# Performance work log

Hardware: AMD Instinct MI355X
Metric: run time of the kernel (lower is better)

The kernel has to match this reference:

```python
import jax, jax.numpy as jnp
import numpy as np

B, S, D, H = 2, 2048, 1024, 16
HD = D // H

def setup_inputs() -> dict:
    key = jax.random.key(0)
    ks = jax.random.split(key, 12)
    std = 1.0 / np.sqrt(D)
    query = jax.random.normal(ks[0], (B, S, D), jnp.float32)
    kk = jax.random.normal(ks[1], (B, S, D), jnp.float32)
    vv = jax.random.normal(ks[2], (B, S, D), jnp.float32)
    # per-batch valid lengths; True = padded position
    lengths = jax.random.randint(ks[3], (B,), S // 2, S + 1)
    key_padding_mask = jnp.arange(S)[None, :] >= lengths[:, None]
    Wq = jax.random.uniform(ks[4], (D, D), jnp.float32, -std, std)
    bq = jnp.zeros((D,), jnp.float32)
    Wk = jax.random.uniform(ks[5], (D, D), jnp.float32, -std, std)
    bk = jnp.zeros((D,), jnp.float32)
    Wv = jax.random.uniform(ks[6], (D, D), jnp.float32, -std, std)
    bv = jnp.zeros((D,), jnp.float32)
    Wo = jax.random.uniform(ks[7], (D, D), jnp.float32, -std, std)
    bo = jnp.zeros((D,), jnp.float32)
    return {"query": query, "key": kk, "value": vv,
            "key_padding_mask": key_padding_mask,
            "Wq": Wq, "bq": bq, "Wk": Wk, "bk": bk,
            "Wv": Wv, "bv": bv, "Wo": Wo, "bo": bo}

def reference(query, key, value, key_padding_mask, Wq, bq, Wk, bk, Wv, bv, Wo, bo):
    scale = HD ** -0.5
    # projections -> [B, H, S, HD]
    def proj(x, W, b):
        return (x @ W.T + b).reshape(B, S, H, HD).transpose(0, 2, 1, 3)
    q = proj(query, Wq, bq)
    k = proj(key, Wk, bk)
    v = proj(value, Wv, bv)
    scores = jnp.einsum('bhqd,bhkd->bhqk', q, k) * scale  # [B,H,S,S]
    pos = jnp.arange(S)
    rel_bias = -0.1 * jnp.abs(pos[:, None] - pos[None, :]).astype(scores.dtype)
    scores = scores + rel_bias[None, None]
    scores = jnp.where(key_padding_mask[:, None, None, :], -jnp.inf, scores)
    attn = jax.nn.softmax(scores, axis=-1)  # dropout is identity in eval
    out = jnp.einsum('bhqk,bhkd->bhqd', attn, v)
    out = out.transpose(0, 2, 1, 3).reshape(B, S, D)
    return out @ Wo.T + bo
```

## Files before the change

kernel.cpp:

```cpp
#include <hip/hip_runtime.h>

typedef __attribute__((ext_vector_type(8))) short bf16x8;
typedef __attribute__((ext_vector_type(4))) short s16x4;
typedef __attribute__((ext_vector_type(8))) short s16x8;
typedef __attribute__((ext_vector_type(4))) float fx4;
typedef __attribute__((ext_vector_type(2))) unsigned int u32x2;

static __device__ __forceinline__ short f2bf(float f) {
  unsigned u = __builtin_bit_cast(unsigned, f);
  u += 0x7fffu + ((u >> 16) & 1u);
  return (short)(u >> 16);
}

static __device__ __forceinline__ void gload_lds16(const void* g, void* l) {
  __builtin_amdgcn_global_load_lds(
      (const __attribute__((address_space(1))) unsigned int*)g,
      (__attribute__((address_space(3))) unsigned int*)l, 16, 0, 0);
}

#define BB_ 2
#define SS_ 2048
#define DD_ 1024
#define HH_ 16
#define HD_ 64

__global__ __launch_bounds__(256) void cvt_kernel(
    const float* __restrict__ q, const float* __restrict__ k, const float* __restrict__ v,
    const float* __restrict__ Wq, const float* __restrict__ Wk, const float* __restrict__ Wv,
    const float* __restrict__ Wo,
    short* __restrict__ xq, short* __restrict__ xk, short* __restrict__ xv,
    short* __restrict__ wq, short* __restrict__ wk, short* __restrict__ wv,
    short* __restrict__ wo) {
  size_t e = ((size_t)blockIdx.x * 256 + threadIdx.x) * 8;
  const float* src; short* dst; size_t off;
  if (e < 4194304u)        { src = q;  dst = xq; off = e; }
  else if (e < 8388608u)   { src = k;  dst = xk; off = e - 4194304u; }
  else if (e < 12582912u)  { src = v;  dst = xv; off = e - 8388608u; }
  else if (e < 13631488u)  { src = Wq; dst = wq; off = e - 12582912u; }
  else if (e < 14680064u)  { src = Wk; dst = wk; off = e - 13631488u; }
  else if (e < 15728640u)  { src = Wv; dst = wv; off = e - 14680064u; }
  else                     { src = Wo; dst = wo; off = e - 15728640u; }
  fx4 a = *(const fx4*)(src + off);
  fx4 b = *(const fx4*)(src + off + 4);
  s16x8 o;
  o[0] = f2bf(a[0]); o[1] = f2bf(a[1]); o[2] = f2bf(a[2]); o[3] = f2bf(a[3]);
  o[4] = f2bf(b[0]); o[5] = f2bf(b[1]); o[6] = f2bf(b[2]); o[7] = f2bf(b[3]);
  *(s16x8*)(dst + off) = o;
}

__global__ __launch_bounds__(256) void proj_gemm(
    const short* __restrict__ xq, const short* __restrict__ xk, const short* __restrict__ xv,
    const short* __restrict__ wq, const short* __restrict__ wk, const short* __restrict__ wv,
    const float* __restrict__ bq, const float* __restrict__ bk, const float* __restrict__ bv,
    short* __restrict__ qout, short* __restrict__ kout, short* __restrict__ vtout) {
  constexpr int K = DD_;
  __shared__ short As[2][128 * 32];
  __shared__ short Bs[2][128 * 32];
  int z = blockIdx.z;
  const short* A = (z == 0) ? xq : ((z == 1) ? xk : xv);
  const short* W = (z == 0) ? wq : ((z == 1) ? wk : wv);
  const float* bias = (z == 0) ? bq : ((z == 1) ? bk : bv);
  int m0 = blockIdx.x * 128, n0 = blockIdx.y * 128;
  int tid = threadIdx.x, lane = tid & 63, wv_ = tid >> 6;
  int wr = wv_ >> 1, wc = wv_ & 1;
  int c = lane & 15, g = lane >> 4;
  fx4 acc[4][4] = {};

  const char* Ab = (const char*)A + (size_t)m0 * K * 2;
  const char* Wb = (const char*)W + (size_t)n0 * K * 2;
  int o0 = tid * 16, o1 = (256 + tid) * 16;
  size_t aoff0 = (size_t)(o0 >> 6) * (K * 2) + (o0 & 63);
  size_t aoff1 = (size_t)(o1 >> 6) * (K * 2) + (o1 & 63);

  gload_lds16(Ab + aoff0, ((char*)As[0]) + o0);
  gload_lds16(Ab + aoff1, ((char*)As[0]) + o1);
  gload_lds16(Wb + aoff0, ((char*)Bs[0]) + o0);
  gload_lds16(Wb + aoff1, ((char*)Bs[0]) + o1);
  __syncthreads();

  for (int k0 = 0; k0 < K; k0 += 32) {
    int cur = (k0 >> 5) & 1;
    if (k0 + 32 < K) {
      size_t kb2 = (size_t)(k0 + 32) * 2;
      gload_lds16(Ab + aoff0 + kb2, ((char*)As[cur ^ 1]) + o0);
      gload_lds16(Ab + aoff1 + kb2, ((char*)As[cur ^ 1]) + o1);
      gload_lds16(Wb + aoff0 + kb2, ((char*)Bs[cur ^ 1]) + o0);
      gload_lds16(Wb + aoff1 + kb2, ((char*)Bs[cur ^ 1]) + o1);
    }
    bf16x8 a[4], b[4];
#pragma unroll
    for (int i = 0; i < 4; i++) a[i] = *(const bf16x8*)(As[cur] + (wr * 64 + i * 16 + c) * 32 + g * 8);
#pragma unroll
    for (int j = 0; j < 4; j++) b[j] = *(const bf16x8*)(Bs[cur] + (wc * 64 + j * 16 + c) * 32 + g * 8);
#pragma unroll
    for (int i = 0; i < 4; i++)
#pragma unroll
      for (int j = 0; j < 4; j++)
        acc[i][j] = __builtin_amdgcn_mfma_f32_16x16x32_bf16(a[i], b[j], acc[i][j], 0, 0, 0);
    __syncthreads();
  }

#pragma unroll
  for (int i = 0; i < 4; i++)
#pragma unroll
    for (int j = 0; j < 4; j++) {
      int gcol = n0 + wc * 64 + j * 16 + c;
      float bv_ = bias[gcol];
      int hh = gcol >> 6, hd = gcol & 63;
      if (z == 2) {
        int grow0 = m0 + wr * 64 + i * 16 + g * 4;
        int bb2 = grow0 >> 11, s0 = grow0 & 2047;
        s16x4 pk;
#pragma unroll
        for (int r = 0; r < 4; r++) pk[r] = f2bf(acc[i][j][r] + bv_);
        *(s16x4*)(vtout + ((size_t)((bb2 * HH_ + hh) * HD_ + hd) * SS_ + s0)) = pk;
      } else {
#pragma unroll
        for (int r = 0; r < 4; r++) {
          int grow = m0 + wr * 64 + i * 16 + g * 4 + r;
          int bb2 = grow >> 11, s = grow & 2047;
          float val = acc[i][j][r] + bv_;
          size_t idx = ((size_t)(bb2 * HH_ + hh) * SS_ + s) * HD_ + hd;
          if (z == 0) qout[idx] = f2bf(val * 0.1803368801f);
          else        kout[idx] = f2bf(val);
        }
      }
    }
}

__global__ __launch_bounds__(256) void attn_kernel(
    const short* __restrict__ qb, const short* __restrict__ kb, const short* __restrict__ vt,
    const int* __restrict__ mask, short* __restrict__ aout) {
  __shared__ char Ksh[2][8192];
  __shared__ char Vsh[2][8192];
  __shared__ char Plds[4][2048];

  int L = blockIdx.x;
  int W = (L & 7) * 128 + (L >> 3);
  int qblk = W & 31, h = (W >> 5) & 15, b = W >> 9;

  int tid = threadIdx.x, lane = tid & 63, w = tid >> 6;
  int c = lane & 15, g = lane >> 4;

  const char* Kp = (const char*)(kb + (size_t)(b * HH_ + h) * SS_ * HD_);
  const char* Vp = (const char*)(vt + (size_t)(b * HH_ + h) * HD_ * SS_);

  int r8 = lane >> 3, c8 = lane & 7;
  int swz = (c8 ^ r8) * 16;
  int iA = w * 2, iB = w * 2 + 1;
  int kOffA = (iA * 8 + r8) * 128 + swz;
  int kOffB = (iB * 8 + r8) * 128 + swz;
  int vOffA = (iA * 8 + r8) * 4096 + swz;
  int vOffB = (iB * 8 + r8) * 4096 + swz;

  gload_lds16(Kp + kOffA, &Ksh[0][iA * 1024]);
  gload_lds16(Kp + kOffB, &Ksh[0][iB * 1024]);
  gload_lds16(Vp + vOffA, &Vsh[0][iA * 1024]);
  gload_lds16(Vp + vOffB, &Vsh[0][iB * 1024]);

  int lmin = SS_;
  for (int i = lane; i < SS_; i += 64)
    if (mask[b * SS_ + i] && i < lmin) lmin = i;
#pragma unroll
  for (int off = 32; off >= 1; off >>= 1) {
    int o2 = __shfl_xor(lmin, off);
    lmin = (o2 < lmin) ? o2 : lmin;
  }
  int len = lmin;
  int nt = (len + 63) >> 6;
  float lenf = (float)len;

  __syncthreads();

  int q0 = qblk * 64 + w * 16;
  const short* Qp = qb + (size_t)(b * HH_ + h) * SS_ * HD_;
  bf16x8 aq0 = *(const bf16x8*)(Qp + (q0 + c) * HD_ + g * 8);
  bf16x8 aq1 = *(const bf16x8*)(Qp + (q0 + c) * HD_ + 32 + g * 8);
  fx4 o[4] = {};
  fx4 o5 = {};
  float qf = (float)(q0 + c);
  char* Pw = Plds[w];
  const float NB = -0.144269504f;
  int cs = c & 7;
  int rc0 = (g ^ cs) * 16;
  int rc1 = ((4 + g) ^ cs) * 16;
  bf16x8 vones;
#pragma unroll
  for (int i = 0; i < 8; i++) vones[i] = (short)0x3F80;

  for (int t = 0; t < nt; ++t) {
    int cur = t & 1;
    if (t + 1 < nt) {
      const char* kpp = Kp + (t + 1) * 8192;
      const char* vpp = Vp + (t + 1) * 128;
      gload_lds16(kpp + kOffA, &Ksh[cur ^ 1][iA * 1024]);
      gload_lds16(kpp + kOffB, &Ksh[cur ^ 1][iB * 1024]);
      gload_lds16(vpp + vOffA, &Vsh[cur ^ 1][iA * 1024]);
      gload_lds16(vpp + vOffB, &Vsh[cur ^ 1][iB * 1024]);
    }
    const char* Kc = Ksh[cur];
    const char* Vc = Vsh[cur];

    fx4 s[4];
    __builtin_amdgcn_s_setprio(1);
#pragma unroll
    for (int tt = 0; tt < 4; tt++) {
      bf16x8 ak0 = *(const bf16x8*)(Kc + (tt * 16 + c) * 128 + rc0);
      bf16x8 ak1 = *(const bf16x8*)(Kc + (tt * 16 + c) * 128 + rc1);
      fx4 z4 = {};
      s[tt] = __builtin_amdgcn_mfma_f32_16x16x32_bf16(ak0, aq0, z4, 0, 0, 0);
      s[tt] = __builtin_amdgcn_mfma_f32_16x16x32_bf16(ak1, aq1, s[tt], 0, 0, 0);
    }
    __builtin_amdgcn_s_setprio(0);

    float p[16];
    float dq = qf - (float)(t * 64 + g * 4);
#pragma unroll
    for (int tt = 0; tt < 4; tt++)
#pragma unroll
      for (int r = 0; r < 4; r++)
        p[tt * 4 + r] = fmaf(NB, fabsf(dq - (float)(tt * 16 + r)), s[tt][r]);
    if (t == nt - 1) {
      float kvb = (float)(t * 64 + g * 4);
#pragma unroll
      for (int tt = 0; tt < 4; tt++)
#pragma unroll
        for (int r = 0; r < 4; r++)
          if (kvb + (float)(tt * 16 + r) >= lenf) p[tt * 4 + r] = -1e30f;
    }
#pragma unroll
    for (int i = 0; i < 16; i++) p[i] = __builtin_amdgcn_exp2f(p[i]);

#pragma unroll
    for (int tt = 0; tt < 4; tt++) {
      u32x2 pk2;
      pk2[0] = __builtin_amdgcn_perm(__builtin_bit_cast(unsigned, p[tt * 4 + 1]),
                                     __builtin_bit_cast(unsigned, p[tt * 4 + 0]), 0x07060302u);
      pk2[1] = __builtin_amdgcn_perm(__builtin_bit_cast(unsigned, p[tt * 4 + 3]),
                                     __builtin_bit_cast(unsigned, p[tt * 4 + 2]), 0x07060302u);
      *(u32x2*)(Pw + c * 128 + ((2 * tt + (g >> 1)) ^ cs) * 16 + (g & 1) * 8) = pk2;
    }
    bf16x8 pa0 = *(const bf16x8*)(Pw + c * 128 + rc0);
    bf16x8 pa1 = *(const bf16x8*)(Pw + c * 128 + rc1);
    __builtin_amdgcn_s_setprio(1);
#pragma unroll
    for (int n = 0; n < 4; n++) {
      bf16x8 v0 = *(const bf16x8*)(Vc + (n * 16 + c) * 128 + rc0);
      bf16x8 v1 = *(const bf16x8*)(Vc + (n * 16 + c) * 128 + rc1);
      o[n] = __builtin_amdgcn_mfma_f32_16x16x32_bf16(pa0, v0, o[n], 0, 0, 0);
      o[n] = __builtin_amdgcn_mfma_f32_16x16x32_bf16(pa1, v1, o[n], 0, 0, 0);
    }
    o5 = __builtin_amdgcn_mfma_f32_16x16x32_bf16(pa0, vones, o5, 0, 0, 0);
    o5 = __builtin_amdgcn_mfma_f32_16x16x32_bf16(pa1, vones, o5, 0, 0, 0);
    __builtin_amdgcn_s_setprio(0);

    __syncthreads();
  }

  float linv[4];
#pragma unroll
  for (int r = 0; r < 4; r++) linv[r] = 1.0f / o5[r];
#pragma unroll
  for (int n = 0; n < 4; n++)
#pragma unroll
    for (int r = 0; r < 4; r++) {
      int qrow = q0 + g * 4 + r;
      float val = o[n][r] * linv[r];
      aout[((size_t)(b * SS_ + qrow)) * DD_ + h * HD_ + n * 16 + c] = f2bf(val);
    }
}

__global__ __launch_bounds__(256) void oproj_gemm(
    const short* __restrict__ A, const short* __restrict__ W,
    const float* __restrict__ bias, float* __restrict__ out) {
  constexpr int K = DD_;
  __shared__ short As[2][128 * 32];
  __shared__ short Bs[2][128 * 32];
  int m0 = blockIdx.x * 128, n0 = blockIdx.y * 128;
  int tid = threadIdx.x, lane = tid & 63, wv_ = tid >> 6;
  int wr = wv_ >> 1, wc = wv_ & 1;
  int c = lane & 15, g = lane >> 4;
  fx4 acc[4][4] = {};
  const char* Ab = (const char*)A + (size_t)m0 * K * 2;
  const char* Wb = (const char*)W + (size_t)n0 * K * 2;
  int o0 = tid * 16, o1 = (256 + tid) * 16;
  size_t aoff0 = (size_t)(o0 >> 6) * (K * 2) + (o0 & 63);
  size_t aoff1 = (size_t)(o1 >> 6) * (K * 2) + (o1 & 63);

  gload_lds16(Ab + aoff0, ((char*)As[0]) + o0);
  gload_lds16(Ab + aoff1, ((char*)As[0]) + o1);
  gload_lds16(Wb + aoff0, ((char*)Bs[0]) + o0);
  gload_lds16(Wb + aoff1, ((char*)Bs[0]) + o1);
  __syncthreads();

  for (int k0 = 0; k0 < K; k0 += 32) {
    int cur = (k0 >> 5) & 1;
    if (k0 + 32 < K) {
      size_t kb2 = (size_t)(k0 + 32) * 2;
      gload_lds16(Ab + aoff0 + kb2, ((char*)As[cur ^ 1]) + o0);
      gload_lds16(Ab + aoff1 + kb2, ((char*)As[cur ^ 1]) + o1);
      gload_lds16(Wb + aoff0 + kb2, ((char*)Bs[cur ^ 1]) + o0);
      gload_lds16(Wb + aoff1 + kb2, ((char*)Bs[cur ^ 1]) + o1);
    }
    bf16x8 a[4], b[4];
#pragma unroll
    for (int i = 0; i < 4; i++) a[i] = *(const bf16x8*)(As[cur] + (wr * 64 + i * 16 + c) * 32 + g * 8);
#pragma unroll
    for (int j = 0; j < 4; j++) b[j] = *(const bf16x8*)(Bs[cur] + (wc * 64 + j * 16 + c) * 32 + g * 8);
#pragma unroll
    for (int i = 0; i < 4; i++)
#pragma unroll
      for (int j = 0; j < 4; j++)
        acc[i][j] = __builtin_amdgcn_mfma_f32_16x16x32_bf16(a[i], b[j], acc[i][j], 0, 0, 0);
    __syncthreads();
  }

#pragma unroll
  for (int i = 0; i < 4; i++)
#pragma unroll
    for (int j = 0; j < 4; j++) {
      int gcol = n0 + wc * 64 + j * 16 + c;
      float bv_ = bias[gcol];
#pragma unroll
      for (int r = 0; r < 4; r++) {
        int grow = m0 + wr * 64 + i * 16 + g * 4 + r;
        out[(size_t)grow * DD_ + gcol] = acc[i][j][r] + bv_;
      }
    }
}

extern "C" void kernel_launch(void* const* d_in, const int* in_sizes, int n_in,
                              void* d_out, int out_size, void* d_ws, size_t ws_size,
                              hipStream_t stream) {
  const float* q  = (const float*)d_in[0];
  const float* k  = (const float*)d_in[1];
  const float* v  = (const float*)d_in[2];
  const int* mask = (const int*)d_in[3];
  const float* Wq = (const float*)d_in[4];
  const float* bq = (const float*)d_in[5];
  const float* Wk = (const float*)d_in[6];
  const float* bk = (const float*)d_in[7];
  const float* Wv = (const float*)d_in[8];
  const float* bv = (const float*)d_in[9];
  const float* Wo = (const float*)d_in[10];
  const float* bo = (const float*)d_in[11];

  char* ws = (char*)d_ws;
  short* qbuf = (short*)(ws);
  short* kbuf = (short*)(ws + (8ull << 20));
  short* vtb  = (short*)(ws + (16ull << 20));
  short* abuf = (short*)(ws + (24ull << 20));
  short* xq   = (short*)(ws + (32ull << 20));
  short* xk   = (short*)(ws + (40ull << 20));
  short* xv   = (short*)(ws + (48ull << 20));
  short* wq   = (short*)(ws + (56ull << 20));
  short* wk   = (short*)(ws + (58ull << 20));
  short* wv   = (short*)(ws + (60ull << 20));
  short* wo   = (short*)(ws + (62ull << 20));
  float* out  = (float*)d_out;

  cvt_kernel<<<8192, 256, 0, stream>>>(q, k, v, Wq, Wk, Wv, Wo, xq, xk, xv, wq, wk, wv, wo);
  dim3 gp(32, 8, 3);
  proj_gemm<<<gp, 256, 0, stream>>>(xq, xk, xv, wq, wk, wv, bq, bk, bv, qbuf, kbuf, vtb);
  attn_kernel<<<1024, 256, 0, stream>>>(qbuf, kbuf, vtb, mask, abuf);
  dim3 go(32, 8, 1);
  oproj_gemm<<<go, 256, 0, stream>>>(abuf, wo, bo, out);
}
```

Before: 229.0 us.

## Give attention waves two query groups and halve oproj M tile

The attention kernel now runs 2 waves per block instead of 4, with each wave handling 32 query rows (two 16-row groups). Each wave reuses every K/V fragment it loads from LDS across both groups, which halves LDS reads per MFMA, and each wave issues four global-to-LDS loads per tile instead of two. Separately, the output projection GEMM shrinks its M tile from 128 to 64, doubling the grid to 512 blocks for better CU occupancy at the cost of reloading the weight tiles more often. The cost is higher register pressure in attention and fewer waves per block available to hide latency.

```diff
diff --git a/kernel.cpp b/kernel.cpp
--- a/kernel.cpp
+++ b/kernel.cpp
@@ -128,12 +128,12 @@
     }
 }
 
-__global__ __launch_bounds__(256) void attn_kernel(
+__global__ __launch_bounds__(128) void attn_kernel(
     const short* __restrict__ qb, const short* __restrict__ kb, const short* __restrict__ vt,
     const int* __restrict__ mask, short* __restrict__ aout) {
   __shared__ char Ksh[2][8192];
   __shared__ char Vsh[2][8192];
-  __shared__ char Plds[4][2048];
+  __shared__ char Plds[2][4096];
 
   int L = blockIdx.x;
   int W = (L & 7) * 128 + (L >> 3);
@@ -147,16 +147,18 @@
 
   int r8 = lane >> 3, c8 = lane & 7;
   int swz = (c8 ^ r8) * 16;
-  int iA = w * 2, iB = w * 2 + 1;
-  int kOffA = (iA * 8 + r8) * 128 + swz;
-  int kOffB = (iB * 8 + r8) * 128 + swz;
-  int vOffA = (iA * 8 + r8) * 4096 + swz;
-  int vOffB = (iB * 8 + r8) * 4096 + swz;
-
-  gload_lds16(Kp + kOffA, &Ksh[0][iA * 1024]);
-  gload_lds16(Kp + kOffB, &Ksh[0][iB * 1024]);
-  gload_lds16(Vp + vOffA, &Vsh[0][iA * 1024]);
-  gload_lds16(Vp + vOffB, &Vsh[0][iB * 1024]);
+  int kOff[4], vOff[4], ldst[4];
+#pragma unroll
+  for (int j = 0; j < 4; j++) {
+    int i = w * 4 + j;
+    kOff[j] = (i * 8 + r8) * 128 + swz;
+    vOff[j] = (i * 8 + r8) * 4096 + swz;
+    ldst[j] = i * 1024;
+  }
+#pragma unroll
+  for (int j = 0; j < 4; j++) gload_lds16(Kp + kOff[j], &Ksh[0][ldst[j]]);
+#pragma unroll
+  for (int j = 0; j < 4; j++) gload_lds16(Vp + vOff[j], &Vsh[0][ldst[j]]);
 
   int lmin = SS_;
   for (int i = lane; i < SS_; i += 64)
@@ -172,13 +174,17 @@
 
   __syncthreads();
 
-  int q0 = qblk * 64 + w * 16;
+  int q0w = qblk * 64 + w * 32;
   const short* Qp = qb + (size_t)(b * HH_ + h) * SS_ * HD_;
-  bf16x8 aq0 = *(const bf16x8*)(Qp + (q0 + c) * HD_ + g * 8);
-  bf16x8 aq1 = *(const bf16x8*)(Qp + (q0 + c) * HD_ + 32 + g * 8);
-  fx4 o[4] = {};
-  fx4 o5 = {};
-  float qf = (float)(q0 + c);
+  bf16x8 aq[2][2];
+#pragma unroll
+  for (int qg = 0; qg < 2; qg++) {
+    aq[qg][0] = *(const bf16x8*)(Qp + (q0w + qg * 16 + c) * HD_ + g * 8);
+    aq[qg][1] = *(const bf16x8*)(Qp + (q0w + qg * 16 + c) * HD_ + 32 + g * 8);
+  }
+  fx4 o[2][4] = {};
+  fx4 o5[2] = {};
+  float qf0 = (float)(q0w + c);
   char* Pw = Plds[w];
   const float NB = -0.144269504f;
   int cs = c & 7;
@@ -193,122 +199,142 @@
     if (t + 1 < nt) {
       const char* kpp = Kp + (t + 1) * 8192;
       const char* vpp = Vp + (t + 1) * 128;
-      gload_lds16(kpp + kOffA, &Ksh[cur ^ 1][iA * 1024]);
-      gload_lds16(kpp + kOffB, &Ksh[cur ^ 1][iB * 1024]);
-      gload_lds16(vpp + vOffA, &Vsh[cur ^ 1][iA * 1024]);
-      gload_lds16(vpp + vOffB, &Vsh[cur ^ 1][iB * 1024]);
+#pragma unroll
+      for (int j = 0; j < 4; j++) gload_lds16(kpp + kOff[j], &Ksh[cur ^ 1][ldst[j]]);
+#pragma unroll
+      for (int j = 0; j < 4; j++) gload_lds16(vpp + vOff[j], &Vsh[cur ^ 1][ldst[j]]);
     }
     const char* Kc = Ksh[cur];
     const char* Vc = Vsh[cur];
 
-    fx4 s[4];
+    fx4 s[2][4];
     __builtin_amdgcn_s_setprio(1);
 #pragma unroll
     for (int tt = 0; tt < 4; tt++) {
       bf16x8 ak0 = *(const bf16x8*)(Kc + (tt * 16 + c) * 128 + rc0);
       bf16x8 ak1 = *(const bf16x8*)(Kc + (tt * 16 + c) * 128 + rc1);
-      fx4 z4 = {};
-      s[tt] = __builtin_amdgcn_mfma_f32_16x16x32_bf16(ak0, aq0, z4, 0, 0, 0);
-      s[tt] = __builtin_amdgcn_mfma_f32_16x16x32_bf16(ak1, aq1, s[tt], 0, 0, 0);
+#pragma unroll
+      for (int qg = 0; qg < 2; qg++) {
+        fx4 z4 = {};
+        s[qg][tt] = __builtin_amdgcn_mfma_f32_16x16x32_bf16(ak0, aq[qg][0], z4, 0, 0, 0);
+        s[qg][tt] = __builtin_amdgcn_mfma_f32_16x16x32_bf16(ak1, aq[qg][1], s[qg][tt], 0, 0, 0);
+      }
     }
     __builtin_amdgcn_s_setprio(0);
 
-    float p[16];
-    float dq = qf - (float)(t * 64 + g * 4);
-#pragma unroll
-    for (int tt = 0; tt < 4; tt++)
-#pragma unroll
-      for (int r = 0; r < 4; r++)
-        p[tt * 4 + r] = fmaf(NB, fabsf(dq - (float)(tt * 16 + r)), s[tt][r]);
-    if (t == nt - 1) {
-      float kvb = (float)(t * 64 + g * 4);
+#pragma unroll
+    for (int qg = 0; qg < 2; qg++) {
+      float p[16];
+      float dq = (qf0 + (float)(qg * 16)) - (float)(t * 64 + g * 4);
 #pragma unroll
       for (int tt = 0; tt < 4; tt++)
 #pragma unroll
         for (int r = 0; r < 4; r++)
-          if (kvb + (float)(tt * 16 + r) >= lenf) p[tt * 4 + r] = -1e30f;
-    }
-#pragma unroll
-    for (int i = 0; i < 16; i++) p[i] = __builtin_amdgcn_exp2f(p[i]);
-
-#pragma unroll
-    for (int tt = 0; tt < 4; tt++) {
-      u32x2 pk2;
-      pk2[0] = __builtin_amdgcn_perm(__builtin_bit_cast(unsigned, p[tt * 4 + 1]),
-                                     __builtin_bit_cast(unsigned, p[tt * 4 + 0]), 0x07060302u);
-      pk2[1] = __builtin_amdgcn_perm(__builtin_bit_cast(unsigned, p[tt * 4 + 3]),
-                                     __builtin_bit_cast(unsigned, p[tt * 4 + 2]), 0x07060302u);
-      *(u32x2*)(Pw + c * 128 + ((2 * tt + (g >> 1)) ^ cs) * 16 + (g & 1) * 8) = pk2;
-    }
-    bf16x8 pa0 = *(const bf16x8*)(Pw + c * 128 + rc0);
-    bf16x8 pa1 = *(const bf16x8*)(Pw + c * 128 + rc1);
+          p[tt * 4 + r] = fmaf(NB, fabsf(dq - (float)(tt * 16 + r)), s[qg][tt][r]);
+      if (t == nt - 1) {
+        float kvb = (float)(t * 64 + g * 4);
+#pragma unroll
+        for (int tt = 0; tt < 4; tt++)
+#pragma unroll
+          for (int r = 0; r < 4; r++)
+            if (kvb + (float)(tt * 16 + r) >= lenf) p[tt * 4 + r] = -1e30f;
+      }
+#pragma unroll
+      for (int i = 0; i < 16; i++) p[i] = __builtin_amdgcn_exp2f(p[i]);
+
+#pragma unroll
+      for (int tt = 0; tt < 4; tt++) {
+        u32x2 pk2;
+        pk2[0] = __builtin_amdgcn_perm(__builtin_bit_cast(unsigned, p[tt * 4 + 1]),
+                                       __builtin_bit_cast(unsigned, p[tt * 4 + 0]), 0x07060302u);
+        pk2[1] = __builtin_amdgcn_perm(__builtin_bit_cast(unsigned, p[tt * 4 + 3]),
+                                       __builtin_bit_cast(unsigned, p[tt * 4 + 2]), 0x07060302u);
+        *(u32x2*)(Pw + (qg * 16 + c) * 128 + ((2 * tt + (g >> 1)) ^ cs) * 16 + (g & 1) * 8) = pk2;
+      }
+    }
+
+    bf16x8 pa[2][2];
+#pragma unroll
+    for (int qg = 0; qg < 2; qg++) {
+      pa[qg][0] = *(const bf16x8*)(Pw + (qg * 16 + c) * 128 + rc0);
+      pa[qg][1] = *(const bf16x8*)(Pw + (qg * 16 + c) * 128 + rc1);
+    }
     __builtin_amdgcn_s_setprio(1);
 #pragma unroll
     for (int n = 0; n < 4; n++) {
       bf16x8 v0 = *(const bf16x8*)(Vc + (n * 16 + c) * 128 + rc0);
       bf16x8 v1 = *(const bf16x8*)(Vc + (n * 16 + c) * 128 + rc1);
-      o[n] = __builtin_amdgcn_mfma_f32_16x16x32_bf16(pa0, v0, o[n], 0, 0, 0);
-      o[n] = __builtin_amdgcn_mfma_f32_16x16x32_bf16(pa1, v1, o[n], 0, 0, 0);
-    }
-    o5 = __builtin_amdgcn_mfma_f32_16x16x32_bf16(pa0, vones, o5, 0, 0, 0);
-    o5 = __builtin_amdgcn_mfma_f32_16x16x32_bf16(pa1, vones, o5, 0, 0, 0);
+#pragma unroll
+      for (int qg = 0; qg < 2; qg++) {
+        o[qg][n] = __builtin_amdgcn_mfma_f32_16x16x32_bf16(pa[qg][0], v0, o[qg][n], 0, 0, 0);
+        o[qg][n] = __builtin_amdgcn_mfma_f32_16x16x32_bf16(pa[qg][1], v1, o[qg][n], 0, 0, 0);
+      }
+    }
+#pragma unroll
+    for (int qg = 0; qg < 2; qg++) {
+      o5[qg] = __builtin_amdgcn_mfma_f32_16x16x32_bf16(pa[qg][0], vones, o5[qg], 0, 0, 0);
+      o5[qg] = __builtin_amdgcn_mfma_f32_16x16x32_bf16(pa[qg][1], vones, o5[qg], 0, 0, 0);
+    }
     __builtin_amdgcn_s_setprio(0);
 
     __syncthreads();
   }
 
-  float linv[4];
-#pragma unroll
-  for (int r = 0; r < 4; r++) linv[r] = 1.0f / o5[r];
-#pragma unroll
-  for (int n = 0; n < 4; n++)
-#pragma unroll
-    for (int r = 0; r < 4; r++) {
-      int qrow = q0 + g * 4 + r;
-      float val = o[n][r] * linv[r];
-      aout[((size_t)(b * SS_ + qrow)) * DD_ + h * HD_ + n * 16 + c] = f2bf(val);
-    }
+#pragma unroll
+  for (int qg = 0; qg < 2; qg++) {
+    float linv[4];
+#pragma unroll
+    for (int r = 0; r < 4; r++) linv[r] = 1.0f / o5[qg][r];
+#pragma unroll
+    for (int n = 0; n < 4; n++)
+#pragma unroll
+      for (int r = 0; r < 4; r++) {
+        int qrow = q0w + qg * 16 + g * 4 + r;
+        float val = o[qg][n][r] * linv[r];
+        aout[((size_t)(b * SS_ + qrow)) * DD_ + h * HD_ + n * 16 + c] = f2bf(val);
+      }
+  }
 }
 
 __global__ __launch_bounds__(256) void oproj_gemm(
     const short* __restrict__ A, const short* __restrict__ W,
     const float* __restrict__ bias, float* __restrict__ out) {
   constexpr int K = DD_;
-  __shared__ short As[2][128 * 32];
+  __shared__ short As[2][64 * 32];
   __shared__ short Bs[2][128 * 32];
-  int m0 = blockIdx.x * 128, n0 = blockIdx.y * 128;
+  int m0 = blockIdx.x * 64, n0 = blockIdx.y * 128;
   int tid = threadIdx.x, lane = tid & 63, wv_ = tid >> 6;
   int wr = wv_ >> 1, wc = wv_ & 1;
   int c = lane & 15, g = lane >> 4;
-  fx4 acc[4][4] = {};
+  fx4 acc[2][4] = {};
   const char* Ab = (const char*)A + (size_t)m0 * K * 2;
   const char* Wb = (const char*)W + (size_t)n0 * K * 2;
-  int o0 = tid * 16, o1 = (256 + tid) * 16;
-  size_t aoff0 = (size_t)(o0 >> 6) * (K * 2) + (o0 & 63);
-  size_t aoff1 = (size_t)(o1 >> 6) * (K * 2) + (o1 & 63);
-
-  gload_lds16(Ab + aoff0, ((char*)As[0]) + o0);
-  gload_lds16(Ab + aoff1, ((char*)As[0]) + o1);
-  gload_lds16(Wb + aoff0, ((char*)Bs[0]) + o0);
-  gload_lds16(Wb + aoff1, ((char*)Bs[0]) + o1);
+  int oA = tid * 16;
+  int oB0 = tid * 16, oB1 = (256 + tid) * 16;
+  size_t aoffA = (size_t)(oA >> 6) * (K * 2) + (oA & 63);
+  size_t boff0 = (size_t)(oB0 >> 6) * (K * 2) + (oB0 & 63);
+  size_t boff1 = (size_t)(oB1 >> 6) * (K * 2) + (oB1 & 63);
+
+  gload_lds16(Ab + aoffA, ((char*)As[0]) + oA);
+  gload_lds16(Wb + boff0, ((char*)Bs[0]) + oB0);
+  gload_lds16(Wb + boff1, ((char*)Bs[0]) + oB1);
   __syncthreads();
 
   for (int k0 = 0; k0 < K; k0 += 32) {
     int cur = (k0 >> 5) & 1;
     if (k0 + 32 < K) {
       size_t kb2 = (size_t)(k0 + 32) * 2;
-      gload_lds16(Ab + aoff0 + kb2, ((char*)As[cur ^ 1]) + o0);
-      gload_lds16(Ab + aoff1 + kb2, ((char*)As[cur ^ 1]) + o1);
-      gload_lds16(Wb + aoff0 + kb2, ((char*)Bs[cur ^ 1]) + o0);
-      gload_lds16(Wb + aoff1 + kb2, ((char*)Bs[cur ^ 1]) + o1);
-    }
-    bf16x8 a[4], b[4];
-#pragma unroll
-    for (int i = 0; i < 4; i++) a[i] = *(const bf16x8*)(As[cur] + (wr * 64 + i * 16 + c) * 32 + g * 8);
+      gload_lds16(Ab + aoffA + kb2, ((char*)As[cur ^ 1]) + oA);
+      gload_lds16(Wb + boff0 + kb2, ((char*)Bs[cur ^ 1]) + oB0);
+      gload_lds16(Wb + boff1 + kb2, ((char*)Bs[cur ^ 1]) + oB1);
+    }
+    bf16x8 a[2], b[4];
+#pragma unroll
+    for (int i = 0; i < 2; i++) a[i] = *(const bf16x8*)(As[cur] + (wr * 32 + i * 16 + c) * 32 + g * 8);
 #pragma unroll
     for (int j = 0; j < 4; j++) b[j] = *(const bf16x8*)(Bs[cur] + (wc * 64 + j * 16 + c) * 32 + g * 8);
 #pragma unroll
-    for (int i = 0; i < 4; i++)
+    for (int i = 0; i < 2; i++)
 #pragma unroll
       for (int j = 0; j < 4; j++)
         acc[i][j] = __builtin_amdgcn_mfma_f32_16x16x32_bf16(a[i], b[j], acc[i][j], 0, 0, 0);
@@ -316,14 +342,14 @@
   }
 
 #pragma unroll
-  for (int i = 0; i < 4; i++)
+  for (int i = 0; i < 2; i++)
 #pragma unroll
     for (int j = 0; j < 4; j++) {
       int gcol = n0 + wc * 64 + j * 16 + c;
       float bv_ = bias[gcol];
 #pragma unroll
       for (int r = 0; r < 4; r++) {
-        int grow = m0 + wr * 64 + i * 16 + g * 4 + r;
+        int grow = m0 + wr * 32 + i * 16 + g * 4 + r;
         out[(size_t)grow * DD_ + gcol] = acc[i][j][r] + bv_;
       }
     }
@@ -362,7 +388,7 @@
   cvt_kernel<<<8192, 256, 0, stream>>>(q, k, v, Wq, Wk, Wv, Wo, xq, xk, xv, wq, wk, wv, wo);
   dim3 gp(32, 8, 3);
   proj_gemm<<<gp, 256, 0, stream>>>(xq, xk, xv, wq, wk, wv, bq, bk, bv, qbuf, kbuf, vtb);
-  attn_kernel<<<1024, 256, 0, stream>>>(qbuf, kbuf, vtb, mask, abuf);
-  dim3 go(32, 8, 1);
+  attn_kernel<<<1024, 128, 0, stream>>>(qbuf, kbuf, vtb, mask, abuf);
+  dim3 go(64, 8, 1);
   oproj_gemm<<<go, 256, 0, stream>>>(abuf, wo, bo, out);
 }
```

New measurement: 233.9 us. 1.02x slower.
